# Performance work log

Hardware: AMD Instinct MI355X
Metric: run time of the kernel (lower is better)

## Reference

```python
import jax, jax.numpy as jnp
import numpy as np

N = 262144       # batch rows
C = 256          # in_channels
K = 256          # uint8 code range


def setup_inputs() -> dict:
    key = jax.random.key(0)
    k1, k2, k3, k4 = jax.random.split(key, 4)
    left = jax.random.randint(k1, (N, C), 0, K, dtype=jnp.int32)
    right = jax.random.randint(k2, (N, C), 0, K, dtype=jnp.int32)
    # per-channel 256x256 lookup tables: white_table[c][l, r] -> new code in [0, 256)
    white_table = jax.random.randint(k3, (C, K, K), 0, K, dtype=jnp.int32)
    # per-channel last-layer codebook: last_codebook[c][1][code] -> float
    codebook = jax.random.normal(k4, (C, K), dtype=jnp.float32)
    return {"left": left, "right": right, "white_table": white_table, "codebook": codebook}


def reference(left, right, white_table, codebook):
    # Fused equivalent of the per-channel python loop:
    #   for c: codes[:, c] = white_table[c][left[:, c], right[:, c]]
    #   out[:, c]  = codebook[c][codes[:, c]]
    ch = jnp.arange(C, dtype=jnp.int32)[None, :]          # [1, C] broadcasts vs [N, C]
    codes = white_table[ch, left, right]                   # [N, C] int32 gather
    out = codebook[ch, codes]                              # [N, C] float32 gather
    return out
```

## Files before the change

### kernel.cpp

```cpp
#include <hip/hip_runtime.h>
#include <stdint.h>

#define CCH 256
#define KK  256

typedef int   i32x4 __attribute__((ext_vector_type(4)));
typedef float f32x4 __attribute__((ext_vector_type(4)));
typedef unsigned short u16x4 __attribute__((ext_vector_type(4)));
typedef unsigned short u16x8 __attribute__((ext_vector_type(8)));

__global__ __launch_bounds__(256) void compress_table_kernel(
    const int4* __restrict__ t, uchar4* __restrict__ o, int n4) {
  int i = blockIdx.x * 256 + threadIdx.x;
  if (i < n4) {
    int4 v = t[i];
    o[i] = make_uchar4((unsigned char)v.x, (unsigned char)v.y,
                       (unsigned char)v.z, (unsigned char)v.w);
  }
}

__global__ __launch_bounds__(512, 4) void transpose_pack_kernel(
    const i32x4* __restrict__ L4, const i32x4* __restrict__ R4,
    unsigned short* __restrict__ LRt, int n0_base, int nslice) {
  __shared__ unsigned short tile[128 * 260];
  const int tn  = blockIdx.x;
  const int gn0 = n0_base + tn * 128;

#pragma unroll
  for (int p = 0; p < 16; ++p) {
    const int idx = p * 512 + (int)threadIdx.x;
    const int r   = idx >> 6;
    const int cq  = idx & 63;
    const size_t gi = (size_t)(gn0 + r) * 64 + cq;
    i32x4 Lv = L4[gi];
    i32x4 Rv = R4[gi];
    u16x4 w;
    w[0] = (unsigned short)((Lv[0] << 8) | Rv[0]);
    w[1] = (unsigned short)((Lv[1] << 8) | Rv[1]);
    w[2] = (unsigned short)((Lv[2] << 8) | Rv[2]);
    w[3] = (unsigned short)((Lv[3] << 8) | Rv[3]);
    const int col = (cq * 4) ^ (((r >> 3) & 15) << 2);
    *(u16x4*)&tile[r * 260 + col] = w;
  }
  __syncthreads();

  const int wv = threadIdx.x >> 6;
  const int l  = threadIdx.x & 63;
  const int m  = l & 15;
  const int c4 = l >> 4;
#pragma unroll
  for (int p = 0; p < 8; ++p) {
    const int ch = wv * 32 + p * 4 + c4;
    u16x8 v;
#pragma unroll
    for (int j = 0; j < 8; ++j) {
      const int r = m * 8 + j;
      v[j] = tile[r * 260 + (ch ^ (m << 2))];
    }
    *(u16x8*)&LRt[(size_t)ch * nslice + (size_t)tn * 128 + m * 8] = v;
  }
}

__global__ __launch_bounds__(512, 4) void code_gather_kernel(
    const unsigned short* __restrict__ LRt, const unsigned char* __restrict__ tab8,
    unsigned char* __restrict__ codes, int nslice) {
  __shared__ unsigned char tabs[KK * KK];
  const int c   = blockIdx.x & (CCH - 1);
  const int sub = blockIdx.x >> 8;
  const size_t base = (size_t)c * nslice + (size_t)sub * 32768;
  const u16x8* __restrict__ in   = (const u16x8*)(LRt + base);
  uint2*       __restrict__ outp = (uint2*)(codes + base);

  u16x8 v0 = in[0 * 512 + threadIdx.x];
  u16x8 v1 = in[1 * 512 + threadIdx.x];
  u16x8 v2 = in[2 * 512 + threadIdx.x];
  u16x8 v3 = in[3 * 512 + threadIdx.x];
  u16x8 v4 = in[4 * 512 + threadIdx.x];
  u16x8 v5 = in[5 * 512 + threadIdx.x];
  u16x8 v6 = in[6 * 512 + threadIdx.x];
  u16x8 v7 = in[7 * 512 + threadIdx.x];

  {
    const int4* src = (const int4*)(tab8 + (size_t)c * (KK * KK));
    int4* dst = (int4*)tabs;
#pragma unroll
    for (int i = 0; i < 8; ++i) dst[i * 512 + threadIdx.x] = src[i * 512 + threadIdx.x];
  }
  __syncthreads();

#define PACK8(v, slot)                                                          \
  {                                                                             \
    unsigned lo = (unsigned)tabs[v[0]] | ((unsigned)tabs[v[1]] << 8) |          \
                  ((unsigned)tabs[v[2]] << 16) | ((unsigned)tabs[v[3]] << 24);  \
    unsigned hi = (unsigned)tabs[v[4]] | ((unsigned)tabs[v[5]] << 8) |          \
                  ((unsigned)tabs[v[6]] << 16) | ((unsigned)tabs[v[7]] << 24);  \
    outp[slot * 512 + threadIdx.x] = make_uint2(lo, hi);                        \
  }
  PACK8(v0, 0) PACK8(v1, 1) PACK8(v2, 2) PACK8(v3, 3)
  PACK8(v4, 4) PACK8(v5, 5) PACK8(v6, 6) PACK8(v7, 7)
#undef PACK8
}

__global__ __launch_bounds__(512, 2) void codebook_transpose_kernel(
    const unsigned char* __restrict__ codes, const float* __restrict__ cb,
    float* __restrict__ out, int n0_base, int nslice) {
  __shared__ float    cbs[64 * KK];
  __shared__ unsigned ctile[64 * 129];
  const int cg = blockIdx.x & 3;
  const int tn = blockIdx.x >> 2;
  const int c0 = cg * 64;

  {
    const f32x4* cbg = (const f32x4*)(cb + (size_t)c0 * KK);
    f32x4* cbl = (f32x4*)cbs;
#pragma unroll
    for (int i = 0; i < 8; ++i) cbl[i * 512 + threadIdx.x] = cbg[i * 512 + threadIdx.x];
  }
  {
    const int cc = threadIdx.x >> 3;
    const int s  = threadIdx.x & 7;
    const unsigned char* srow = codes + (size_t)(c0 + cc) * nslice + (size_t)tn * 512;
#pragma unroll
    for (int k = 0; k < 4; ++k) {
      uint4 val = *(const uint4*)(srow + s * 16 + k * 128);
      const int d0 = cc * 129 + k * 32 + s * 4;
      ctile[d0 + 0] = val.x;
      ctile[d0 + 1] = val.y;
      ctile[d0 + 2] = val.z;
      ctile[d0 + 3] = val.w;
    }
  }
  __syncthreads();

  const int l = threadIdx.x & 63;
  const int w = threadIdx.x >> 6;
  const float* cbrow = cbs + l * KK;
  float* ob = out + (size_t)(n0_base + tn * 512) * CCH + c0 + l;
#pragma unroll
  for (int it = 0; it < 16; ++it) {
    const int n4 = it * 8 + w;
    const unsigned cw = ctile[l * 129 + n4];
#pragma unroll
    for (int k = 0; k < 4; ++k) {
      const float vv = cbrow[(cw >> (8 * k)) & 255u];
      __builtin_nontemporal_store(vv, ob + (size_t)(n4 * 4 + k) * CCH);
    }
  }
}

#define ROWS_PER_BLOCK 512
#define NGROUPS 16
#define GCH (CCH / NGROUPS)

template <typename TabT>
__global__ __launch_bounds__(256, 8) void gather_kernel(
    const i32x4* __restrict__ left, const i32x4* __restrict__ right,
    const TabT* __restrict__ tab, const float* __restrict__ cb,
    f32x4* __restrict__ out, int nrows) {
  __shared__ float cbs[GCH * KK];
  const int g     = blockIdx.x & (NGROUPS - 1);
  const int chunk = blockIdx.x / NGROUPS;
  const int q     = threadIdx.x & 3;
  const int rsub  = threadIdx.x >> 2;
  {
    const f32x4* cbg = (const f32x4*)(cb + (size_t)(g * GCH) * KK);
    f32x4* cbl = (f32x4*)cbs;
#pragma unroll
    for (int i = 0; i < 4; ++i) cbl[threadIdx.x + i * 256] = cbg[threadIdx.x + i * 256];
  }
  __syncthreads();
  const int cbase  = g * GCH + q * 4;
  const TabT* t0   = tab + (size_t)cbase * (KK * KK);
  const int vecoff = g * 4 + q;
  const float* cq  = cbs + (q * 4) * KK;
  const int rbase = chunk * ROWS_PER_BLOCK;
#pragma unroll
  for (int it = 0; it < ROWS_PER_BLOCK / 32; ++it) {
    const int r0 = rbase + it * 32 + rsub;
    if (r0 >= nrows) break;
    const unsigned v0 = (unsigned)r0 * 64u + (unsigned)vecoff;
    i32x4 L0 = left[v0];
    i32x4 R0 = right[v0];
    unsigned c0 = (unsigned)t0[          (unsigned)(L0[0] * KK + R0[0])];
    unsigned c1 = (unsigned)t0[ 65536u + (unsigned)(L0[1] * KK + R0[1])];
    unsigned c2 = (unsigned)t0[131072u + (unsigned)(L0[2] * KK + R0[2])];
    unsigned c3 = (unsigned)t0[196608u + (unsigned)(L0[3] * KK + R0[3])];
    f32x4 o;
    o[0] = cq[       c0];
    o[1] = cq[KK   + c1];
    o[2] = cq[2*KK + c2];
    o[3] = cq[3*KK + c3];
    out[v0] = o;
  }
}

extern "C" void kernel_launch(void* const* d_in, const int* in_sizes, int n_in,
                              void* d_out, int out_size, void* d_ws, size_t ws_size,
                              hipStream_t stream) {
  const int*   left  = (const int*)d_in[0];
  const int*   right = (const int*)d_in[1];
  const int*   wt    = (const int*)d_in[2];
  const float* cb    = (const float*)d_in[3];
  float* out = (float*)d_out;

  const int nrows = in_sizes[0] / CCH;
  const int tab_elems = CCH * KK * KK;
  const size_t tab_bytes = (size_t)tab_elems;

  int S = 0;
  for (int s = 1; s <= 8; s <<= 1) {
    if (nrows % (s * 32768)) continue;
    size_t need = tab_bytes + (size_t)768 * (size_t)(nrows / s);
    if (need <= ws_size) { S = s; break; }
  }

  if (S) {
    unsigned char* tab8 = (unsigned char*)d_ws;
    int n4 = tab_elems / 4;
    compress_table_kernel<<<n4 / 256, 256, 0, stream>>>(
        (const int4*)wt, (uchar4*)tab8, n4);

    const int nslice = nrows / S;
    unsigned short* LRt = (unsigned short*)((char*)d_ws + tab_bytes);
    unsigned char* codes = (unsigned char*)d_ws + tab_bytes + (size_t)512 * nslice;

    for (int h = 0; h < S; ++h) {
      const int n0 = h * nslice;
      transpose_pack_kernel<<<nslice / 128, 512, 0, stream>>>(
          (const i32x4*)left, (const i32x4*)right, LRt, n0, nslice);
      code_gather_kernel<<<(nslice / 32768) * CCH, 512, 0, stream>>>(
          LRt, tab8, codes, nslice);
      codebook_transpose_kernel<<<(nslice / 512) * 4, 512, 0, stream>>>(
          codes, cb, out, n0, nslice);
    }
  } else if (ws_size >= tab_bytes) {
    unsigned char* tab8 = (unsigned char*)d_ws;
    int n4 = tab_elems / 4;
    compress_table_kernel<<<n4 / 256, 256, 0, stream>>>(
        (const int4*)wt, (uchar4*)tab8, n4);
    const int blocks = ((nrows + ROWS_PER_BLOCK - 1) / ROWS_PER_BLOCK) * NGROUPS;
    gather_kernel<unsigned char><<<blocks, 256, 0, stream>>>(
        (const i32x4*)left, (const i32x4*)right, tab8, cb, (f32x4*)out, nrows);
  } else {
    const int blocks = ((nrows + ROWS_PER_BLOCK - 1) / ROWS_PER_BLOCK) * NGROUPS;
    gather_kernel<int><<<blocks, 256, 0, stream>>>(
        (const i32x4*)left, (const i32x4*)right, wt, cb, (f32x4*)out, nrows);
  }
}
```

Before: 709.8 us.

## Use direct global-to-LDS table loads, shrink codebook tiles, prefer 4 slices

The per-channel table staging in code_gather_kernel now uses global_load_lds, which moves data straight from global memory into LDS without passing through registers. codebook_transpose_kernel is restructured to handle 32 channels by 256 rows per block. This cuts LDS use so that six blocks can fit per CU, and each thread now writes full float4 vectors across four channels instead of scalar stores. The slice count now prefers S=4 ahead of S=1, trading launch count for workspace locality and L2 reuse of the intermediates.

```diff
diff --git a/kernel.cpp b/kernel.cpp
--- a/kernel.cpp
+++ b/kernel.cpp
@@ -8,6 +8,12 @@
 typedef float f32x4 __attribute__((ext_vector_type(4)));
 typedef unsigned short u16x4 __attribute__((ext_vector_type(4)));
 typedef unsigned short u16x8 __attribute__((ext_vector_type(8)));
+
+typedef const __attribute__((address_space(1))) void gas_t;
+typedef __attribute__((address_space(3))) void las_t;
+__device__ __forceinline__ void gl_lds16(const void* g, void* l) {
+  __builtin_amdgcn_global_load_lds((gas_t*)g, (las_t*)l, 16, 0, 0);
+}
 
 __global__ __launch_bounds__(256) void compress_table_kernel(
     const int4* __restrict__ t, uchar4* __restrict__ o, int n4) {
@@ -67,84 +73,82 @@
   __shared__ unsigned char tabs[KK * KK];
   const int c   = blockIdx.x & (CCH - 1);
   const int sub = blockIdx.x >> 8;
+  const int tid = threadIdx.x;
   const size_t base = (size_t)c * nslice + (size_t)sub * 32768;
-  const u16x8* __restrict__ in   = (const u16x8*)(LRt + base);
-  uint2*       __restrict__ outp = (uint2*)(codes + base);
-
-  u16x8 v0 = in[0 * 512 + threadIdx.x];
-  u16x8 v1 = in[1 * 512 + threadIdx.x];
-  u16x8 v2 = in[2 * 512 + threadIdx.x];
-  u16x8 v3 = in[3 * 512 + threadIdx.x];
-  u16x8 v4 = in[4 * 512 + threadIdx.x];
-  u16x8 v5 = in[5 * 512 + threadIdx.x];
-  u16x8 v6 = in[6 * 512 + threadIdx.x];
-  u16x8 v7 = in[7 * 512 + threadIdx.x];
-
-  {
-    const int4* src = (const int4*)(tab8 + (size_t)c * (KK * KK));
-    int4* dst = (int4*)tabs;
-#pragma unroll
-    for (int i = 0; i < 8; ++i) dst[i * 512 + threadIdx.x] = src[i * 512 + threadIdx.x];
-  }
-  __syncthreads();
-
-#define PACK8(v, slot)                                                          \
-  {                                                                             \
-    unsigned lo = (unsigned)tabs[v[0]] | ((unsigned)tabs[v[1]] << 8) |          \
-                  ((unsigned)tabs[v[2]] << 16) | ((unsigned)tabs[v[3]] << 24);  \
-    unsigned hi = (unsigned)tabs[v[4]] | ((unsigned)tabs[v[5]] << 8) |          \
-                  ((unsigned)tabs[v[6]] << 16) | ((unsigned)tabs[v[7]] << 24);  \
-    outp[slot * 512 + threadIdx.x] = make_uint2(lo, hi);                        \
-  }
-  PACK8(v0, 0) PACK8(v1, 1) PACK8(v2, 2) PACK8(v3, 3)
-  PACK8(v4, 4) PACK8(v5, 5) PACK8(v6, 6) PACK8(v7, 7)
-#undef PACK8
-}
-
-__global__ __launch_bounds__(512, 2) void codebook_transpose_kernel(
+  const u16x8* __restrict__ in = (const u16x8*)(LRt + base);
+
+  u16x8 v[8];
+#pragma unroll
+  for (int i = 0; i < 8; ++i) v[i] = in[i * 512 + tid];
+
+  {
+    const int w = tid >> 6, lane = tid & 63;
+    const unsigned char* tsrc = tab8 + (size_t)c * (KK * KK) + w * 8192 + lane * 16;
+    unsigned int* tdst = (unsigned int*)tabs + w * 2048;
+#pragma unroll
+    for (int i = 0; i < 8; ++i) gl_lds16(tsrc + i * 1024, tdst + i * 256);
+  }
+  __syncthreads();
+
+  uint2* outp = (uint2*)(codes + base);
+#pragma unroll
+  for (int i = 0; i < 8; ++i) {
+    unsigned lo = (unsigned)tabs[v[i][0]] | ((unsigned)tabs[v[i][1]] << 8) |
+                  ((unsigned)tabs[v[i][2]] << 16) | ((unsigned)tabs[v[i][3]] << 24);
+    unsigned hi = (unsigned)tabs[v[i][4]] | ((unsigned)tabs[v[i][5]] << 8) |
+                  ((unsigned)tabs[v[i][6]] << 16) | ((unsigned)tabs[v[i][7]] << 24);
+    outp[i * 512 + tid] = make_uint2(lo, hi);
+  }
+}
+
+__global__ __launch_bounds__(512, 6) void codebook_transpose_kernel(
     const unsigned char* __restrict__ codes, const float* __restrict__ cb,
     float* __restrict__ out, int n0_base, int nslice) {
-  __shared__ float    cbs[64 * KK];
-  __shared__ unsigned ctile[64 * 129];
-  const int cg = blockIdx.x & 3;
-  const int tn = blockIdx.x >> 2;
-  const int c0 = cg * 64;
+  __shared__ float    cbs[32 * KK];
+  __shared__ unsigned ctd[32 * 65];
+  const int cg = blockIdx.x & 7;
+  const int tn = blockIdx.x >> 3;
+  const int c0 = cg * 32;
+  const int tid = threadIdx.x;
 
   {
     const f32x4* cbg = (const f32x4*)(cb + (size_t)c0 * KK);
     f32x4* cbl = (f32x4*)cbs;
 #pragma unroll
-    for (int i = 0; i < 8; ++i) cbl[i * 512 + threadIdx.x] = cbg[i * 512 + threadIdx.x];
-  }
-  {
-    const int cc = threadIdx.x >> 3;
-    const int s  = threadIdx.x & 7;
-    const unsigned char* srow = codes + (size_t)(c0 + cc) * nslice + (size_t)tn * 512;
-#pragma unroll
-    for (int k = 0; k < 4; ++k) {
-      uint4 val = *(const uint4*)(srow + s * 16 + k * 128);
-      const int d0 = cc * 129 + k * 32 + s * 4;
-      ctile[d0 + 0] = val.x;
-      ctile[d0 + 1] = val.y;
-      ctile[d0 + 2] = val.z;
-      ctile[d0 + 3] = val.w;
-    }
-  }
-  __syncthreads();
-
-  const int l = threadIdx.x & 63;
-  const int w = threadIdx.x >> 6;
-  const float* cbrow = cbs + l * KK;
-  float* ob = out + (size_t)(n0_base + tn * 512) * CCH + c0 + l;
-#pragma unroll
-  for (int it = 0; it < 16; ++it) {
-    const int n4 = it * 8 + w;
-    const unsigned cw = ctile[l * 129 + n4];
-#pragma unroll
-    for (int k = 0; k < 4; ++k) {
-      const float vv = cbrow[(cw >> (8 * k)) & 255u];
-      __builtin_nontemporal_store(vv, ob + (size_t)(n4 * 4 + k) * CCH);
-    }
+    for (int i = 0; i < 4; ++i) cbl[i * 512 + tid] = cbg[i * 512 + tid];
+  }
+  {
+    const int cc = tid >> 4;
+    const int s  = tid & 15;
+    const uint4 val = *(const uint4*)(codes + (size_t)(c0 + cc) * nslice +
+                                      (size_t)tn * 256 + s * 16);
+    const int d0 = cc * 65 + s * 4;
+    ctd[d0 + 0] = val.x;
+    ctd[d0 + 1] = val.y;
+    ctd[d0 + 2] = val.z;
+    ctd[d0 + 3] = val.w;
+  }
+  __syncthreads();
+
+  const int cq = tid & 7;
+  const int nb = tid >> 3;
+  const unsigned cw0 = ctd[(cq * 4 + 0) * 65 + nb];
+  const unsigned cw1 = ctd[(cq * 4 + 1) * 65 + nb];
+  const unsigned cw2 = ctd[(cq * 4 + 2) * 65 + nb];
+  const unsigned cw3 = ctd[(cq * 4 + 3) * 65 + nb];
+  const float* b0 = cbs + (cq * 4 + 0) * KK;
+  const float* b1 = cbs + (cq * 4 + 1) * KK;
+  const float* b2 = cbs + (cq * 4 + 2) * KK;
+  const float* b3 = cbs + (cq * 4 + 3) * KK;
+  float* ob = out + (size_t)(n0_base + tn * 256 + nb * 4) * CCH + c0 + cq * 4;
+#pragma unroll
+  for (int k = 0; k < 4; ++k) {
+    f32x4 o;
+    o[0] = b0[(cw0 >> (8 * k)) & 255u];
+    o[1] = b1[(cw1 >> (8 * k)) & 255u];
+    o[2] = b2[(cw2 >> (8 * k)) & 255u];
+    o[3] = b3[(cw3 >> (8 * k)) & 255u];
+    __builtin_nontemporal_store(o, (f32x4*)(ob + (size_t)k * CCH));
   }
 }
 
@@ -208,10 +212,14 @@
   const size_t tab_bytes = (size_t)tab_elems;
 
   int S = 0;
-  for (int s = 1; s <= 8; s <<= 1) {
-    if (nrows % (s * 32768)) continue;
-    size_t need = tab_bytes + (size_t)768 * (size_t)(nrows / s);
-    if (need <= ws_size) { S = s; break; }
+  {
+    const int prefs[5] = {4, 8, 16, 2, 1};
+    for (int pi = 0; pi < 5; ++pi) {
+      const int s = prefs[pi];
+      if (nrows % (s * 32768)) continue;
+      size_t need = tab_bytes + (size_t)768 * (size_t)(nrows / s);
+      if (need <= ws_size) { S = s; break; }
+    }
   }
 
   if (S) {
@@ -230,7 +238,7 @@
           (const i32x4*)left, (const i32x4*)right, LRt, n0, nslice);
       code_gather_kernel<<<(nslice / 32768) * CCH, 512, 0, stream>>>(
           LRt, tab8, codes, nslice);
-      codebook_transpose_kernel<<<(nslice / 512) * 4, 512, 0, stream>>>(
+      codebook_transpose_kernel<<<(nslice / 256) * 8, 512, 0, stream>>>(
           codes, cb, out, n0, nslice);
     }
   } else if (ws_size >= tab_bytes) {
```

New measurement: 704.6 us. No clear change (-0.7%).
